# Kernel tuning notes

Hardware: AMD Instinct MI355X
Metric: run time of the kernel (lower is better)

## Reference

```python
import jax, jax.numpy as jnp
import numpy as np

HEADS = 16
SCALE = 8.0
EPS = 1e-12  # F.normalize eps for fp32


def _l2norm(t):
    # F.normalize(t, dim=-1): t / max(||t||, eps)
    n = jnp.sqrt(jnp.sum(t * t, axis=-1, keepdims=True))
    return t / jnp.maximum(n, EPS)


def setup_inputs() -> dict:
    key = jax.random.key(0)
    k0, k1, k2, k3, k4 = jax.random.split(key, 5)
    b, n, d = 1, 4096, 1024
    w_scale = 1.0 / np.sqrt(d)
    return {
        "x": jax.random.normal(k0, (b, n, d), dtype=jnp.float32),
        "Wq": jax.random.normal(k1, (d, d), dtype=jnp.float32) * w_scale,
        "Wk": jax.random.normal(k2, (d, d), dtype=jnp.float32) * w_scale,
        "Wv": jax.random.normal(k3, (d, d), dtype=jnp.float32) * w_scale,
        "Wo": jax.random.normal(k4, (d, d), dtype=jnp.float32) * w_scale,
    }


def reference(x, Wq, Wk, Wv, Wo):
    b, n, d = x.shape
    h = HEADS
    dh = d // h
    # projections (nn.Linear without bias): y = x @ W  (W stored as [in, out])
    def proj(W):
        y = jnp.einsum('bnd,df->bnf', x, W)
        return y.reshape(b, n, h, dh).transpose(0, 2, 1, 3)  # b h n dh
    q, k, v = proj(Wq), proj(Wk), proj(Wv)
    # cosine-sim attention: L2-normalize q, k along head dim
    q = _l2norm(q)
    k = _l2norm(k)
    sim = jnp.einsum('bhid,bhjd->bhij', q, k) * SCALE
    mask_value = -jnp.finfo(sim.dtype).max
    causal = jnp.triu(jnp.ones((n, n), dtype=bool), 1)
    sim = jnp.where(causal, mask_value, sim)
    attn = jax.nn.softmax(sim, axis=-1)
    o = jnp.einsum('bhij,bhjd->bhid', attn, v)
    o = o.transpose(0, 2, 1, 3).reshape(b, n, d)  # b n (h dh)
    return jnp.einsum('bnf,fd->bnd', o, Wo)
```

## Files before the change

kernel.cpp:

```cpp
#include <hip/hip_runtime.h>
#include <stdint.h>
#include <math.h>

typedef __bf16 bf16_t;
typedef __attribute__((ext_vector_type(8))) __bf16 bf16x8;
typedef __attribute__((ext_vector_type(4))) __bf16 bf16x4;
typedef __attribute__((ext_vector_type(4))) float f32x4;

#define N_TOK 4096
#define D_MODEL 1024
#define HEADS 16
#define DH 64
#define C1 11.541560327111707f
#define C2 11.721897207207671f

__device__ __forceinline__ void async_copy16(const void* g, void* l) {
    __builtin_amdgcn_global_load_lds(
        (const __attribute__((address_space(1))) unsigned int*)g,
        (__attribute__((address_space(3))) unsigned int*)l, 16, 0, 0);
}

__global__ __launch_bounds__(256) void cast_x_kernel(const float* __restrict__ x,
                                                     bf16_t* __restrict__ xb) {
    int i = (blockIdx.x * 256 + threadIdx.x) * 4;
    float4 v = *(const float4*)(x + i);
    bf16x4 o;
    o[0] = (bf16_t)v.x; o[1] = (bf16_t)v.y; o[2] = (bf16_t)v.z; o[3] = (bf16_t)v.w;
    *(bf16x4*)(xb + i) = o;
}

__global__ __launch_bounds__(256) void transpose_w_kernel(
    const float* __restrict__ W0, const float* __restrict__ W1,
    const float* __restrict__ W2, const float* __restrict__ W3,
    bf16_t* __restrict__ T0, bf16_t* __restrict__ T1,
    bf16_t* __restrict__ T2, bf16_t* __restrict__ T3) {
    __shared__ bf16_t t[64][72];
    const float* W; bf16_t* T;
    switch (blockIdx.z) {
        case 0: W = W0; T = T0; break;
        case 1: W = W1; T = T1; break;
        case 2: W = W2; T = T2; break;
        default: W = W3; T = T3; break;
    }
    int k0 = blockIdx.x * 64, n0 = blockIdx.y * 64;
    int tx = threadIdx.x & 63, ty = threadIdx.x >> 6;
#pragma unroll
    for (int i = 0; i < 16; i++) {
        int kl = ty * 16 + i;
        t[kl][tx] = (bf16_t)W[(size_t)(k0 + kl) * D_MODEL + n0 + tx];
    }
    __syncthreads();
#pragma unroll
    for (int i = 0; i < 16; i++) {
        int nl = ty * 16 + i;
        T[(size_t)(n0 + nl) * D_MODEL + k0 + tx] = t[tx][nl];
    }
}

template <int WRITE_F32, int NORM>
__global__ __launch_bounds__(256) void gemm_tile(const bf16_t* __restrict__ A,
                                                 const bf16_t* __restrict__ Bt,
                                                 void* __restrict__ Cout, int ldc) {
    constexpr int K = D_MODEL;
    __shared__ __align__(16) bf16_t As[128 * 32];
    __shared__ __align__(16) bf16_t Bs[128 * 32];
    const int tid = threadIdx.x;
    const int m0 = blockIdx.y * 128;
    const int n0 = blockIdx.x * 128;
    const int wave = tid >> 6;
    const int lane = tid & 63;
    const int l15 = lane & 15;
    const int quad = lane >> 4;
    const int wm = (wave >> 1) * 64;
    const int wn = (wave & 1) * 64;
    f32x4 acc[4][4] = {};

    const int srow = tid >> 2;
    const int soff = (tid & 3) * 8;
    const bf16_t* gA = A + (size_t)(m0 + srow) * K + soff;
    const bf16_t* gB = Bt + (size_t)(n0 + srow) * K + soff;
    bf16_t* lA = &As[tid * 8];
    bf16_t* lB = &Bs[tid * 8];
    constexpr int HGAP = 64 * K;

    for (int kt = 0; kt < K; kt += 32) {
        __syncthreads();
        async_copy16(gA + kt, lA);
        async_copy16(gA + HGAP + kt, lA + 2048);
        async_copy16(gB + kt, lB);
        async_copy16(gB + HGAP + kt, lB + 2048);
        __syncthreads();
        bf16x8 af[4], bfr[4];
#pragma unroll
        for (int mi = 0; mi < 4; mi++)
            af[mi] = *(const bf16x8*)(&As[(wm + mi * 16 + l15) * 32 + quad * 8]);
#pragma unroll
        for (int ni = 0; ni < 4; ni++)
            bfr[ni] = *(const bf16x8*)(&Bs[(wn + ni * 16 + l15) * 32 + quad * 8]);
#pragma unroll
        for (int mi = 0; mi < 4; mi++)
#pragma unroll
            for (int ni = 0; ni < 4; ni++)
                acc[mi][ni] = __builtin_amdgcn_mfma_f32_16x16x32_bf16(
                    af[mi], bfr[ni], acc[mi][ni], 0, 0, 0);
    }

    if (NORM && n0 < 2048) {
#pragma unroll
        for (int mi = 0; mi < 4; mi++)
#pragma unroll
            for (int r = 0; r < 4; r++) {
                float s = 0.f;
#pragma unroll
                for (int ni = 0; ni < 4; ni++) {
                    float v = acc[mi][ni][r];
                    s += v * v;
                }
                s += __shfl_xor(s, 1);
                s += __shfl_xor(s, 2);
                s += __shfl_xor(s, 4);
                s += __shfl_xor(s, 8);
                float sc = 1.0f / fmaxf(sqrtf(s), 1e-12f);
#pragma unroll
                for (int ni = 0; ni < 4; ni++) acc[mi][ni][r] *= sc;
            }
    }
#pragma unroll
    for (int mi = 0; mi < 4; mi++)
#pragma unroll
        for (int ni = 0; ni < 4; ni++)
#pragma unroll
            for (int r = 0; r < 4; r++) {
                int row = m0 + wm + mi * 16 + quad * 4 + r;
                int col = n0 + wn + ni * 16 + l15;
                float v = acc[mi][ni][r];
                if (WRITE_F32)
                    ((float*)Cout)[(size_t)row * ldc + col] = v;
                else
                    ((bf16_t*)Cout)[(size_t)row * ldc + col] = (bf16_t)v;
            }
}

__global__ __launch_bounds__(256) void transpose_v_kernel(const bf16_t* __restrict__ QKV,
                                                          bf16_t* __restrict__ Vt) {
    __shared__ bf16_t t[64][72];
    int n0 = blockIdx.x * 64;
    int h = blockIdx.y;
    int tx = threadIdx.x & 63, ty = threadIdx.x >> 6;
#pragma unroll
    for (int i = 0; i < 16; i++) {
        int nl = ty * 16 + i;
        t[nl][tx] = QKV[(size_t)(n0 + nl) * 3072 + 2048 + h * DH + tx];
    }
    __syncthreads();
    const int e = tx & 7, q = (tx >> 3) & 3;
    const int J = (tx & 32) + 16 * (e >> 2) + 4 * q + (e & 3);
#pragma unroll
    for (int i = 0; i < 16; i++) {
        int dl = ty * 16 + i;
        Vt[(size_t)(h * DH + dl) * N_TOK + n0 + tx] = t[J][dl];
    }
}

__global__ __launch_bounds__(256) void attn_kernel(const bf16_t* __restrict__ QKV,
                                                   const bf16_t* __restrict__ Vt,
                                                   bf16_t* __restrict__ O) {
    __shared__ __align__(16) bf16_t Ks[2][4096];
    __shared__ __align__(16) bf16_t Vs[2][2][2048];
    const int tid = threadIdx.x;
    const int wave = tid >> 6;
    const int lane = tid & 63;
    const int l15 = lane & 15;
    const int quad = lane >> 4;

    const int xcd = blockIdx.x & 7;
    const int t = blockIdx.x >> 3;
    const int h = xcd * 2 + (t & 1);
    const int g = 63 - (t >> 1);
    const int i0 = g * 64 + wave * 16;

    const bf16_t* Qb = QKV + h * DH;
    const bf16_t* Kb = QKV + 1024 + h * DH;
    const bf16_t* Vb = Vt + (size_t)h * DH * N_TOK;

    bf16x8 aq[2];
#pragma unroll
    for (int kd = 0; kd < 2; kd++)
        aq[kd] = *(const bf16x8*)(Qb + (size_t)(i0 + l15) * 3072 + kd * 32 + quad * 8);

    f32x4 od[4] = {};
    float l_acc = 0.f;

    const int krow = tid >> 3;
    const int kc = (tid & 7) ^ (krow & 7);
    const bf16_t* gK = Kb + (size_t)krow * 3072 + kc * 8;
    const int vd = tid >> 2;
    const int vc = (tid & 3) ^ ((vd >> 1) & 3);
    const bf16_t* gV = Vb + (size_t)vd * N_TOK + vc * 8;

    async_copy16(gK, &Ks[0][tid * 8]);
    async_copy16(gK + (size_t)32 * 3072, &Ks[0][tid * 8 + 2048]);
    async_copy16(gV, &Vs[0][0][tid * 8]);
    async_copy16(gV + 32, &Vs[0][1][tid * 8]);

    const int ksw = l15 & 7;
    const int vsw = (l15 >> 1) & 3;

    for (int jt = 0; jt <= g; jt++) {
        __syncthreads();
        if (jt < g) {
            const int b = (jt + 1) & 1;
            const bf16_t* kn = gK + (size_t)(jt + 1) * 64 * 3072;
            async_copy16(kn, &Ks[b][tid * 8]);
            async_copy16(kn + (size_t)32 * 3072, &Ks[b][tid * 8 + 2048]);
            async_copy16(gV + (jt + 1) * 64, &Vs[b][0][tid * 8]);
            async_copy16(gV + (jt + 1) * 64 + 32, &Vs[b][1][tid * 8]);
        }
        const bf16_t* KS = Ks[jt & 1];
        const bool diag = (jt == g);
        const int jh_max = diag ? wave : 3;

        bf16x8 ak[4][2];
#pragma unroll
        for (int jh = 0; jh < 4; jh++) {
            if (jh > jh_max) continue;
#pragma unroll
            for (int kd = 0; kd < 2; kd++)
                ak[jh][kd] = *(const bf16x8*)(&KS[(jh * 16 + l15) * 64 +
                                                  (((kd * 4 + quad) ^ ksw) * 8)]);
        }
        f32x4 sj[4] = {};
#pragma unroll
        for (int kd = 0; kd < 2; kd++)
#pragma unroll
            for (int jh = 0; jh < 4; jh++) {
                if (jh > jh_max) continue;
                sj[jh] = __builtin_amdgcn_mfma_f32_16x16x32_bf16(ak[jh][kd], aq[kd], sj[jh], 0, 0, 0);
            }

        float p[4][4] = {};
#pragma unroll
        for (int jh = 0; jh < 4; jh++) {
            if (jh > jh_max) continue;
            if (diag && jh == wave) {
#pragma unroll
                for (int r = 0; r < 4; r++) {
                    float v = (quad * 4 + r > l15) ? 0.f
                              : __builtin_amdgcn_exp2f(sj[jh][r] * C1 - C2);
                    p[jh][r] = v;
                    l_acc += v;
                }
            } else {
#pragma unroll
                for (int r = 0; r < 4; r++) {
                    float v = __builtin_amdgcn_exp2f(sj[jh][r] * C1 - C2);
                    p[jh][r] = v;
                    l_acc += v;
                }
            }
        }
        bf16x8 pk8[2];
#pragma unroll
        for (int H = 0; H < 2; H++)
#pragma unroll
            for (int r = 0; r < 4; r++) {
                pk8[H][r] = (bf16_t)p[2 * H][r];
                pk8[H][4 + r] = (bf16_t)p[2 * H + 1][r];
            }

        const bf16_t* VS0 = Vs[jt & 1][0];
#pragma unroll
        for (int mt = 0; mt < 4; mt++) {
            bf16x8 vf = *(const bf16x8*)(&VS0[(mt * 16 + l15) * 32 + ((quad ^ vsw) * 8)]);
            od[mt] = __builtin_amdgcn_mfma_f32_16x16x32_bf16(vf, pk8[0], od[mt], 0, 0, 0);
        }
        if (jh_max >= 2) {
            const bf16_t* VS1 = Vs[jt & 1][1];
#pragma unroll
            for (int mt = 0; mt < 4; mt++) {
                bf16x8 vf = *(const bf16x8*)(&VS1[(mt * 16 + l15) * 32 + ((quad ^ vsw) * 8)]);
                od[mt] = __builtin_amdgcn_mfma_f32_16x16x32_bf16(vf, pk8[1], od[mt], 0, 0, 0);
            }
        }
    }

    float l = l_acc;
    l += __shfl_xor(l, 16);
    l += __shfl_xor(l, 32);
    float inv = 1.0f / l;

#pragma unroll
    for (int mt = 0; mt < 4; mt++) {
        bf16x4 o;
#pragma unroll
        for (int r = 0; r < 4; r++) o[r] = (bf16_t)(od[mt][r] * inv);
        *(bf16x4*)(&O[(size_t)(i0 + l15) * D_MODEL + h * DH + mt * 16 + quad * 4]) = o;
    }
}

extern "C" void kernel_launch(void* const* d_in, const int* in_sizes, int n_in,
                              void* d_out, int out_size, void* d_ws, size_t ws_size,
                              hipStream_t stream) {
    const float* x  = (const float*)d_in[0];
    const float* Wq = (const float*)d_in[1];
    const float* Wk = (const float*)d_in[2];
    const float* Wv = (const float*)d_in[3];
    const float* Wo = (const float*)d_in[4];
    float* out = (float*)d_out;
    char* ws = (char*)d_ws;
    const size_t MB = 1024 * 1024;
    bf16_t* xb   = (bf16_t*)(ws);
    bf16_t* Wt3  = (bf16_t*)(ws + 8 * MB);
    bf16_t* Wot  = (bf16_t*)(ws + 14 * MB);
    bf16_t* QKV  = (bf16_t*)(ws + 16 * MB);
    bf16_t* Vt   = (bf16_t*)(ws + 40 * MB);
    bf16_t* Ob   = (bf16_t*)(ws + 48 * MB);

    cast_x_kernel<<<4096, 256, 0, stream>>>(x, xb);
    dim3 gw(16, 16, 4);
    transpose_w_kernel<<<gw, 256, 0, stream>>>(Wq, Wk, Wv, Wo,
                                               Wt3, Wt3 + 1024 * 1024, Wt3 + 2 * 1024 * 1024, Wot);
    dim3 gqkv(3072 / 128, N_TOK / 128);
    gemm_tile<0, 1><<<gqkv, 256, 0, stream>>>(xb, Wt3, QKV, 3072);
    dim3 gv(N_TOK / 64, HEADS);
    transpose_v_kernel<<<gv, 256, 0, stream>>>(QKV, Vt);
    attn_kernel<<<1024, 256, 0, stream>>>(QKV, Vt, Ob);
    dim3 go(D_MODEL / 128, N_TOK / 128);
    gemm_tile<1, 0><<<go, 256, 0, stream>>>(Ob, Wot, out, D_MODEL);
}
```

Measured before the change: 210.8 us.

## Merge two adjacent query tiles per 512-thread attention block sharing K/V tiles

Each attention block now has 8 waves covering two consecutive 64-row query tiles (gA=2u+1, gB=2u) of the same head, and both tiles share one double-buffered K/V stream in LDS. Each thread issues half as many async copies per tile, and K/V global traffic per head is roughly halved. Waves on the lower tile skip the last iteration but still take part in the barriers, so they sit idle for that step. The grid is halved to 512 blocks, which lowers the number of blocks in flight and may change occupancy.

```diff
diff --git a/kernel.cpp b/kernel.cpp
--- a/kernel.cpp
+++ b/kernel.cpp
@@ -162,7 +162,7 @@
     }
 }
 
-__global__ __launch_bounds__(256) void attn_kernel(const bf16_t* __restrict__ QKV,
+__global__ __launch_bounds__(512) void attn_kernel(const bf16_t* __restrict__ QKV,
                                                    const bf16_t* __restrict__ Vt,
                                                    bf16_t* __restrict__ O) {
     __shared__ __align__(16) bf16_t Ks[2][4096];
@@ -176,8 +176,12 @@
     const int xcd = blockIdx.x & 7;
     const int t = blockIdx.x >> 3;
     const int h = xcd * 2 + (t & 1);
-    const int g = 63 - (t >> 1);
-    const int i0 = g * 64 + wave * 16;
+    const int u = 31 - (t >> 1);
+    const int gA = 2 * u + 1;
+    const int gB = 2 * u;
+    const int wm = wave & 3;
+    const int g_my = (wave < 4) ? gA : gB;
+    const int i0 = g_my * 64 + wm * 16;
 
     const bf16_t* Qb = QKV + h * DH;
     const bf16_t* Kb = QKV + 1024 + h * DH;
@@ -194,31 +198,29 @@
     const int krow = tid >> 3;
     const int kc = (tid & 7) ^ (krow & 7);
     const bf16_t* gK = Kb + (size_t)krow * 3072 + kc * 8;
-    const int vd = tid >> 2;
-    const int vc = (tid & 3) ^ ((vd >> 1) & 3);
-    const bf16_t* gV = Vb + (size_t)vd * N_TOK + vc * 8;
+    const int vH = tid >> 8;
+    const int vsl = tid & 255;
+    const int vd = vsl >> 2;
+    const int vc = (vsl & 3) ^ ((vd >> 1) & 3);
+    const bf16_t* gV = Vb + (size_t)vd * N_TOK + vc * 8 + vH * 32;
 
     async_copy16(gK, &Ks[0][tid * 8]);
-    async_copy16(gK + (size_t)32 * 3072, &Ks[0][tid * 8 + 2048]);
-    async_copy16(gV, &Vs[0][0][tid * 8]);
-    async_copy16(gV + 32, &Vs[0][1][tid * 8]);
+    async_copy16(gV, &Vs[0][vH][vsl * 8]);
 
     const int ksw = l15 & 7;
     const int vsw = (l15 >> 1) & 3;
 
-    for (int jt = 0; jt <= g; jt++) {
+    for (int jt = 0; jt <= gA; jt++) {
         __syncthreads();
-        if (jt < g) {
+        if (jt < gA) {
             const int b = (jt + 1) & 1;
-            const bf16_t* kn = gK + (size_t)(jt + 1) * 64 * 3072;
-            async_copy16(kn, &Ks[b][tid * 8]);
-            async_copy16(kn + (size_t)32 * 3072, &Ks[b][tid * 8 + 2048]);
-            async_copy16(gV + (jt + 1) * 64, &Vs[b][0][tid * 8]);
-            async_copy16(gV + (jt + 1) * 64 + 32, &Vs[b][1][tid * 8]);
-        }
+            async_copy16(gK + (size_t)(jt + 1) * 64 * 3072, &Ks[b][tid * 8]);
+            async_copy16(gV + (jt + 1) * 64, &Vs[b][vH][vsl * 8]);
+        }
+        if (jt > g_my) continue;
         const bf16_t* KS = Ks[jt & 1];
-        const bool diag = (jt == g);
-        const int jh_max = diag ? wave : 3;
+        const bool diag = (jt == g_my);
+        const int jh_max = diag ? wm : 3;
 
         bf16x8 ak[4][2];
 #pragma unroll
@@ -242,7 +244,7 @@
 #pragma unroll
         for (int jh = 0; jh < 4; jh++) {
             if (jh > jh_max) continue;
-            if (diag && jh == wave) {
+            if (diag && jh == wm) {
 #pragma unroll
                 for (int r = 0; r < 4; r++) {
                     float v = (quad * 4 + r > l15) ? 0.f
@@ -324,7 +326,7 @@
     gemm_tile<0, 1><<<gqkv, 256, 0, stream>>>(xb, Wt3, QKV, 3072);
     dim3 gv(N_TOK / 64, HEADS);
     transpose_v_kernel<<<gv, 256, 0, stream>>>(QKV, Vt);
-    attn_kernel<<<1024, 256, 0, stream>>>(QKV, Vt, Ob);
+    attn_kernel<<<512, 512, 0, stream>>>(QKV, Vt, Ob);
     dim3 go(D_MODEL / 128, N_TOK / 128);
     gemm_tile<1, 0><<<go, 256, 0, stream>>>(Ob, Wot, out, D_MODEL);
 }
```

Measured after the change: 232.4 us. 1.1x slower.
